# Kernel optimization log

Measured on AMD Instinct MI355X. Metric: run time of the kernel, lower is better.

Reference implementation:

```python
import jax, jax.numpy as jnp
import numpy as np

EPS = 1e-4

def setup_inputs() -> dict:
    key = jax.random.key(0)
    x = jax.random.normal(key, (16, 256, 8192), dtype=jnp.float32)
    return {"x": x}

def reference(x):
    # x: [B, C, T]; cumulative (causal) normalization along time axis
    T = x.shape[-1]
    count = jnp.arange(1, T + 1, dtype=x.dtype).reshape(1, 1, T)
    cum_sum = jnp.cumsum(x, axis=-1)
    cum_pow_sum = jnp.cumsum(x * x, axis=-1)
    cum_mean = cum_sum / count
    cum_var = cum_pow_sum / count - cum_mean * cum_mean
    cum_std = jnp.sqrt(cum_var + EPS)
    return (x - cum_mean) / cum_std
```

## Files before the change

kernel.cpp:

```cpp
#include <hip/hip_runtime.h>

#define ROW_T   8192
#define THREADS 256
#define WPB     4
#define NT      32
#define PIPE    12
#define EPSV    1e-4f

typedef float fvec4 __attribute__((ext_vector_type(4)));

template<int CTRL, int RM>
__device__ __forceinline__ float dpp_add(float v) {
    const int p = __builtin_amdgcn_update_dpp(0, __float_as_int(v), CTRL, RM, 0xf, true);
    return v + __int_as_float(p);
}
__device__ __forceinline__ float wave_incl_scan(float v) {
    v = dpp_add<0x111, 0xf>(v);
    v = dpp_add<0x112, 0xf>(v);
    v = dpp_add<0x114, 0xf>(v);
    v = dpp_add<0x118, 0xf>(v);
    v = dpp_add<0x142, 0xa>(v);
    v = dpp_add<0x143, 0xc>(v);
    return v;
}

template<int K>
__device__ __forceinline__ void prologue(const float* __restrict__ pa, fvec4 (&B)[PIPE]) {
    asm volatile("global_load_dwordx4 %0, %1, off" : "=v"(B[K]) : "v"(pa + K * 256));
    if constexpr (K + 1 < PIPE) prologue<K + 1>(pa, B);
}

template<int K>
__device__ __forceinline__ void tile(const float* __restrict__ pa,
                                     float* __restrict__ po,
                                     fvec4 (&B)[PIPE],
                                     float& carry_s, float& carry_ss, const int l4) {
    constexpr int LOADS_AFTER  = (PIPE - 1) < (NT - 1 - K) ? (PIPE - 1) : (NT - 1 - K);
    constexpr int STORES_AFTER = (PIPE < K) ? PIPE : K;
    constexpr int N = LOADS_AFTER + STORES_AFTER;

    asm volatile("s_waitcnt vmcnt(%0)" :: "i"(N));
    __builtin_amdgcn_sched_barrier(0);

    const fvec4 c = B[K % PIPE];

    if constexpr (K + PIPE < NT)
        asm volatile("global_load_dwordx4 %0, %1, off"
                     : "=v"(B[K % PIPE]) : "v"(pa + (K + PIPE) * 256));

    float s  = (c.x + c.y) + (c.z + c.w);
    float ss = fmaf(c.x, c.x, fmaf(c.y, c.y, fmaf(c.z, c.z, c.w * c.w)));

    const float is  = wave_incl_scan(s);
    const float iss = wave_incl_scan(ss);

    float S  = carry_s  + (is  - s);
    float SS = carry_ss + (iss - ss);

    carry_s  += __int_as_float(__builtin_amdgcn_readlane(__float_as_int(is),  63));
    carry_ss += __int_as_float(__builtin_amdgcn_readlane(__float_as_int(iss), 63));

    const int e0 = K * 256 + l4;
    fvec4 o;
#define CN_STEP(v, idx, dst) {                                            \
        S += (v); SS = fmaf((v), (v), SS);                                \
        const float inv  = __builtin_amdgcn_rcpf((float)(e0 + (idx) + 1));\
        const float mean = S * inv;                                       \
        const float var  = fmaf(SS, inv, -(mean * mean));                 \
        (dst) = ((v) - mean) * __builtin_amdgcn_rsqf(var + EPSV);         \
    }
    CN_STEP(c.x, 0, o.x)
    CN_STEP(c.y, 1, o.y)
    CN_STEP(c.z, 2, o.z)
    CN_STEP(c.w, 3, o.w)
#undef CN_STEP

    asm volatile("global_store_dwordx4 %0, %1, off" :: "v"(po + K * 256), "v"(o));

    if constexpr (K + 1 < NT) tile<K + 1>(pa, po, B, carry_s, carry_ss, l4);
}

__global__ __launch_bounds__(THREADS, 4)
void cumnorm_kernel(const float* __restrict__ x, float* __restrict__ out) {
    const int lane = threadIdx.x & 63;
    const int wid  = threadIdx.x >> 6;

    const long long row = (long long)blockIdx.x * WPB + wid;
    const int l4 = lane * 4;
    const float* __restrict__ pa = x   + row * ROW_T + l4;
    float* __restrict__       po = out + row * ROW_T + l4;

    fvec4 B[PIPE];
    prologue<0>(pa, B);

    float carry_s = 0.f, carry_ss = 0.f;
    tile<0>(pa, po, B, carry_s, carry_ss, l4);

    asm volatile("s_waitcnt vmcnt(0)");
}

extern "C" void kernel_launch(void* const* d_in, const int* in_sizes, int n_in,
                              void* d_out, int out_size, void* d_ws, size_t ws_size,
                              hipStream_t stream) {
    const float* x = (const float*)d_in[0];
    float* out = (float*)d_out;
    const int rows = out_size / ROW_T;
    cumnorm_kernel<<<rows / WPB, THREADS, 0, stream>>>(x, out);
}
```

Before: 232.2 us.

## Stage input tiles through LDS via direct global-to-LDS loads

Replaces the register-resident prefetch ring (12 vec4 buffers) with an 8-slot per-wave LDS ring filled by global_load_lds, then reads each tile with ds_read_b128. This is meant to free VGPRs and keep several loads in flight without holding register buffers. In exchange it adds an LDS read and an lgkmcnt wait on every tile, and uses 32KB of LDS per block, which may limit occupancy. It also relies on vmcnt accounting for LDS-direct loads being correct, with a shallower pipeline depth.

Measured after the change: 232.2 us. No clear change (-0.0%).

```diff
diff --git a/kernel.cpp b/kernel.cpp
--- a/kernel.cpp
+++ b/kernel.cpp
@@ -4,10 +4,13 @@
 #define THREADS 256
 #define WPB     4
 #define NT      32
-#define PIPE    12
+#define D       8
+#define SLOT_B  1024
 #define EPSV    1e-4f
 
 typedef float fvec4 __attribute__((ext_vector_type(4)));
+typedef __attribute__((address_space(1))) const float glb_f;
+typedef __attribute__((address_space(3))) float       lds_f;
 
 template<int CTRL, int RM>
 __device__ __forceinline__ float dpp_add(float v) {
@@ -25,28 +28,32 @@
 }
 
 template<int K>
-__device__ __forceinline__ void prologue(const float* __restrict__ pa, fvec4 (&B)[PIPE]) {
-    asm volatile("global_load_dwordx4 %0, %1, off" : "=v"(B[K]) : "v"(pa + K * 256));
-    if constexpr (K + 1 < PIPE) prologue<K + 1>(pa, B);
+__device__ __forceinline__ void prologue_fill(const float* pa, const int lane, char* lwave) {
+    __builtin_amdgcn_global_load_lds((glb_f*)(pa + K * 256 + lane * 4),
+                                     (lds_f*)(lwave + K * SLOT_B), 16, 0, 0);
+    if constexpr (K + 1 < D) prologue_fill<K + 1>(pa, lane, lwave);
 }
 
 template<int K>
-__device__ __forceinline__ void tile(const float* __restrict__ pa,
-                                     float* __restrict__ po,
-                                     fvec4 (&B)[PIPE],
-                                     float& carry_s, float& carry_ss, const int l4) {
-    constexpr int LOADS_AFTER  = (PIPE - 1) < (NT - 1 - K) ? (PIPE - 1) : (NT - 1 - K);
-    constexpr int STORES_AFTER = (PIPE < K) ? PIPE : K;
+__device__ __forceinline__ void tile(const float* pa, float* po, char* lwave,
+                                     float& carry_s, float& carry_ss, const int lane) {
+    constexpr int LOADS_AFTER  = (D - 1) < (NT - 1 - K) ? (D - 1) : (NT - 1 - K);
+    constexpr int STORES_AFTER = (K < D) ? K : D;
     constexpr int N = LOADS_AFTER + STORES_AFTER;
 
     asm volatile("s_waitcnt vmcnt(%0)" :: "i"(N));
     __builtin_amdgcn_sched_barrier(0);
 
-    const fvec4 c = B[K % PIPE];
+    const unsigned loff = (unsigned)(unsigned long long)(lds_f*)(lwave + (K % D) * SLOT_B)
+                        + (unsigned)lane * 16u;
+    fvec4 c;
+    asm volatile("ds_read_b128 %0, %1" : "=v"(c) : "v"(loff));
+    asm volatile("s_waitcnt lgkmcnt(0)");
+    __builtin_amdgcn_sched_barrier(0);
 
-    if constexpr (K + PIPE < NT)
-        asm volatile("global_load_dwordx4 %0, %1, off"
-                     : "=v"(B[K % PIPE]) : "v"(pa + (K + PIPE) * 256));
+    if constexpr (K + D < NT)
+        __builtin_amdgcn_global_load_lds((glb_f*)(pa + (K + D) * 256 + lane * 4),
+                                         (lds_f*)(lwave + (K % D) * SLOT_B), 16, 0, 0);
 
     float s  = (c.x + c.y) + (c.z + c.w);
     float ss = fmaf(c.x, c.x, fmaf(c.y, c.y, fmaf(c.z, c.z, c.w * c.w)));
@@ -60,7 +67,7 @@
     carry_s  += __int_as_float(__builtin_amdgcn_readlane(__float_as_int(is),  63));
     carry_ss += __int_as_float(__builtin_amdgcn_readlane(__float_as_int(iss), 63));
 
-    const int e0 = K * 256 + l4;
+    const int e0 = K * 256 + lane * 4;
     fvec4 o;
 #define CN_STEP(v, idx, dst) {                                            \
         S += (v); SS = fmaf((v), (v), SS);                                \
@@ -77,24 +84,25 @@
 
     asm volatile("global_store_dwordx4 %0, %1, off" :: "v"(po + K * 256), "v"(o));
 
-    if constexpr (K + 1 < NT) tile<K + 1>(pa, po, B, carry_s, carry_ss, l4);
+    if constexpr (K + 1 < NT) tile<K + 1>(pa, po, lwave, carry_s, carry_ss, lane);
 }
 
 __global__ __launch_bounds__(THREADS, 4)
 void cumnorm_kernel(const float* __restrict__ x, float* __restrict__ out) {
+    __shared__ char ldsbuf[WPB * D * SLOT_B];
+
     const int lane = threadIdx.x & 63;
     const int wid  = threadIdx.x >> 6;
 
     const long long row = (long long)blockIdx.x * WPB + wid;
-    const int l4 = lane * 4;
-    const float* __restrict__ pa = x   + row * ROW_T + l4;
-    float* __restrict__       po = out + row * ROW_T + l4;
+    const float* pa = x   + row * ROW_T;
+    float*       po = out + row * ROW_T + lane * 4;
+    char* lwave = ldsbuf + wid * (D * SLOT_B);
 
-    fvec4 B[PIPE];
-    prologue<0>(pa, B);
+    prologue_fill<0>(pa, lane, lwave);
 
     float carry_s = 0.f, carry_ss = 0.f;
-    tile<0>(pa, po, B, carry_s, carry_ss, l4);
+    tile<0>(pa, po, lwave, carry_s, carry_ss, lane);
 
     asm volatile("s_waitcnt vmcnt(0)");
 }
```
